# Optimization experiments

Hardware: AMD Instinct MI355X
Metric: run time of the kernel (lower is better)

The kernel has to match this reference:

```python
import jax, jax.numpy as jnp
from jax import lax
import numpy as np

EPS = 1e-5
BONES = [(0,1),(0,2),(1,3),(2,4),(5,7),(7,9),(6,8),(8,10),(11,13),(13,15),(12,14),(14,16)]


def _build_adj(num_joints=17):
    adj = np.eye(num_joints, dtype=np.float32)
    for i, j in BONES:
        adj[i, j] = 1.0
        adj[j, i] = 1.0
    d = adj.sum(1) ** -0.5
    return jnp.asarray(d[:, None] * adj * d[None, :])


def _bn(x, gamma, beta, axes):
    # training-mode BatchNorm: biased variance over `axes`
    mean = x.mean(axes, keepdims=True)
    var = ((x - mean) ** 2).mean(axes, keepdims=True)
    return (x - mean) * lax.rsqrt(var + EPS) * gamma + beta


def _gcn_block(x, adj, w, b, gamma, beta):
    # x: [N, V, Cin]; adjacency mixing then 1x1 conv (pointwise linear)
    x = jnp.einsum('nvc,vw->nwc', x, adj)
    x = jnp.einsum('nvc,oc->nvo', x, w) + b            # Conv1d(k=1): [N, V, Cout]
    x = _bn(x, gamma, beta, axes=(0, 1))               # BN over channel Cout
    return jax.nn.relu(x)


def setup_inputs() -> dict:
    key = jax.random.key(0)
    ks = jax.random.split(key, 16)
    B, T, V, C, H = 64, 512, 17, 2, 128
    s = 0.1
    return {
        'x':   jax.random.normal(ks[0], (B, T, V, C), jnp.float32),
        'adj': _build_adj(V),
        'w1':  jax.random.normal(ks[1], (64, C), jnp.float32) * s,
        'b1':  jax.random.normal(ks[2], (64,), jnp.float32) * s,
        'g1':  1.0 + jax.random.normal(ks[3], (64,), jnp.float32) * s,
        'be1': jax.random.normal(ks[4], (64,), jnp.float32) * s,
        'w2':  jax.random.normal(ks[5], (H, 64), jnp.float32) * s,
        'b2':  jax.random.normal(ks[6], (H,), jnp.float32) * s,
        'g2':  1.0 + jax.random.normal(ks[7], (H,), jnp.float32) * s,
        'be2': jax.random.normal(ks[8], (H,), jnp.float32) * s,
        'wt':  jax.random.normal(ks[9], (H, H * V, 3), jnp.float32) * 0.02,
        'bt':  jax.random.normal(ks[10], (H,), jnp.float32) * s,
        'gt':  1.0 + jax.random.normal(ks[11], (H,), jnp.float32) * s,
        'bet': jax.random.normal(ks[12], (H,), jnp.float32) * s,
    }


def reference(x, adj, w1, b1, g1, be1, w2, b2, g2, be2, wt, bt, gt, bet):
    B, T, V, C = x.shape
    h = x.reshape(B * T, V, C)
    h = _gcn_block(h, adj, w1, b1, g1, be1)            # [B*T, V, 64]
    h = _gcn_block(h, adj, w2, b2, g2, be2)            # [B*T, V, H]
    H = h.shape[-1]
    # matches torch: view(B,T,V,H).permute(0,3,1,2).contiguous().view(B,-1,T)
    h = h.reshape(B, T, V, H).transpose(0, 3, 1, 2).reshape(B, H * V, T)
    h = lax.conv_general_dilated(h, wt, (1,), [(1, 1)],
                                 dimension_numbers=('NCH', 'OIH', 'NCH'))
    h = h + bt[None, :, None]                          # [B, H, T]
    h = _bn(h, gt[None, :, None], bet[None, :, None], axes=(0, 2))
    h = jax.nn.relu(h)
    return h.transpose(0, 2, 1)                        # [B, T, H]
```

## Files before the change

kernel.cpp:

```cpp
#include <hip/hip_runtime.h>
#include <hip/hip_bf16.h>

#define EPS 1e-5f

static constexpr int Bv = 64, Tv = 512, Vv = 17, Hv = 128;
static constexpr int CHv = Hv * Vv;
static constexpr long ZBv = (long)CHv * Tv;

typedef __attribute__((ext_vector_type(8))) short short8v;
typedef __attribute__((ext_vector_type(4))) float f32x4;
typedef __attribute__((ext_vector_type(4))) int   int4v;

__device__ static const int TAPSP[17] = {
    0 | (1 << 8) | (2 << 16),
    1 | (0 << 8) | (3 << 16),
    2 | (0 << 8) | (4 << 16),
    3 | (1 << 8) | (11 << 16),
    4 | (2 << 8) | (12 << 16),
    5 | (7 << 8) | (13 << 16),
    6 | (8 << 8) | (14 << 16),
    7 | (5 << 8) | (9 << 16),
    8 | (6 << 8) | (10 << 16),
    9 | (7 << 8) | (0 << 16),
    10 | (8 << 8) | (1 << 16),
    11 | (13 << 8) | (2 << 16),
    12 | (14 << 8) | (3 << 16),
    13 | (11 << 8) | (15 << 16),
    14 | (12 << 8) | (16 << 16),
    15 | (13 << 8) | (6 << 16),
    16 | (14 << 8) | (7 << 16),
};

static constexpr size_t SZ_Z    = (size_t)Bv * (size_t)ZBv * 2;
static constexpr size_t OFF_ZR  = 0;
static constexpr size_t OFF_WKT = OFF_ZR + SZ_Z;
static constexpr size_t SZ_WKT  = (size_t)3 * 128 * 2176 * 2;
static constexpr size_t OFF_W2B = OFF_WKT + SZ_WKT;
static constexpr size_t SZ_W2B  = (size_t)128 * 64 * 2;
static constexpr size_t OFF_CP  = OFF_W2B + SZ_W2B;
static constexpr size_t SZ_CP   = (size_t)Bv * Hv * Tv * 4;
static constexpr size_t OFF_ST  = OFF_CP + SZ_CP;

__device__ __forceinline__ int4v ld16(const __hip_bfloat16* p) {
    return *reinterpret_cast<const int4v*>(p);
}
__device__ __forceinline__ f32x4 mfma16(int4v a, int4v b, f32x4 c) {
    return __builtin_amdgcn_mfma_f32_16x16x32_bf16(
        *reinterpret_cast<short8v*>(&a), *reinterpret_cast<short8v*>(&b), c, 0, 0, 0);
}
__device__ __forceinline__ float bf2f(short s) {
    return __uint_as_float(((unsigned)(unsigned short)s) << 16);
}

__global__ __launch_bounds__(256) void k_wt_bf16(const float* __restrict__ wt,
                                                 __hip_bfloat16* __restrict__ wkt2) {
    int i = blockIdx.x * 256 + threadIdx.x;
    if (i >= 3 * 128 * 2176) return;
    int el = i & 7;
    int ln = (i >> 3) & 63;
    int r  = i >> 9;
    int c  = r % 68; r /= 68;
    int oT = r & 7;  int k = r >> 3;
    int o   = oT * 16 + (ln & 15);
    int cip = c * 32 + ((ln >> 4) << 3) + el;
    int q = cip >> 7, o_in = cip & 127;
    wkt2[i] = __float2bfloat16(wt[(size_t)o * 6528 + (o_in * 17 + q) * 3 + k]);
}

__global__ __launch_bounds__(256) void k_w2b(const float* __restrict__ w2,
                                             __hip_bfloat16* __restrict__ w2b) {
    int e = blockIdx.x * 256 + threadIdx.x;
    if (e >= 8192) return;
    w2b[e] = __float2bfloat16(w2[e]);
}

__global__ __launch_bounds__(256) void k_stats1(const float* __restrict__ x,
                                                const float* __restrict__ adj,
                                                const float* __restrict__ w1,
                                                const float* __restrict__ b1,
                                                float* __restrict__ st) {
    __shared__ float adj_s[289];
    __shared__ float xs[32 * 34];
    __shared__ float mix[32 * 34];
    __shared__ float red[256], red2[256];
    int tid = threadIdx.x;
    int n0 = blockIdx.x * 32;
    for (int i = tid; i < 289; i += 256) adj_s[i] = adj[i];
    for (int i = tid; i < 1088; i += 256) xs[i] = x[(size_t)n0 * 34 + i];
    __syncthreads();
    for (int e = tid; e < 1088; e += 256) {
        int n = e / 34, r = e % 34;
        int w = r >> 1, c = r & 1;
        int pk = TAPSP[w];
        float acc = 0.f;
#pragma unroll
        for (int tp = 0; tp < 3; ++tp) {
            int v = (pk >> (8 * tp)) & 31;
            acc += xs[n * 34 + v * 2 + c] * adj_s[v * 17 + w];
        }
        mix[n * 34 + w * 2 + c] = acc;
    }
    __syncthreads();
    int o = tid & 63, g = tid >> 6;
    float w0 = w1[o * 2], w1v = w1[o * 2 + 1], bb = b1[o];
    float s = 0.f, s2 = 0.f;
    for (int n = g; n < 32; n += 4)
        for (int v = 0; v < 17; ++v) {
            float a = mix[n * 34 + v * 2] * w0 + mix[n * 34 + v * 2 + 1] * w1v + bb;
            s += a; s2 += a * a;
        }
    red[tid] = s; red2[tid] = s2;
    __syncthreads();
    if (tid < 64) {
        float S  = red[tid] + red[tid + 64] + red[tid + 128] + red[tid + 192];
        float S2 = red2[tid] + red2[tid + 64] + red2[tid + 128] + red2[tid + 192];
        int slot = blockIdx.x & 15;
        atomicAdd(&st[slot * 64 + o], S);
        atomicAdd(&st[1024 + slot * 64 + o], S2);
    }
}

__global__ void k_finalize(const float* __restrict__ sums, const float* __restrict__ sumsq,
                           const float* __restrict__ gamma, const float* __restrict__ beta,
                           float* __restrict__ scale, float* __restrict__ shift,
                           int count, float inv_denom) {
    int o = threadIdx.x;
    if (o >= count) return;
    float S = 0.f, Q = 0.f;
    for (int j = 0; j < 16; ++j) { S += sums[j * count + o]; Q += sumsq[j * count + o]; }
    float m = S * inv_denom;
    float var = Q * inv_denom - m * m;
    float rstd = rsqrtf(var + EPS);
    float sc = rstd * gamma[o];
    scale[o] = sc;
    shift[o] = beta[o] - m * sc;
}

__global__ __launch_bounds__(256) void k_gcn(const float* __restrict__ x,
                                             const float* __restrict__ adj,
                                             const float* __restrict__ w1,
                                             const float* __restrict__ b1,
                                             const float* __restrict__ sc1,
                                             const float* __restrict__ sh1,
                                             const __hip_bfloat16* __restrict__ w2b,
                                             const float* __restrict__ b2,
                                             float* __restrict__ st,
                                             __hip_bfloat16* __restrict__ zr2) {
    __shared__ float adj_s[289];
    __shared__ float xs[170];
    __shared__ float mix1[170];
    __shared__ __align__(16) char uni[26240];
    __hip_bfloat16* h1b  = reinterpret_cast<__hip_bfloat16*>(uni);
    __hip_bfloat16* m2b  = reinterpret_cast<__hip_bfloat16*>(uni + 14976);
    __hip_bfloat16* a2st = reinterpret_cast<__hip_bfloat16*>(uni);

    int tid = threadIdx.x;
    int bi = blockIdx.x;
    int b = bi / 136, rb = bi - b * 136;
    int r0 = rb * 64;
    int t_lo = r0 / 17;

    for (int i = tid; i < 289; i += 256) adj_s[i] = adj[i];
    for (int i = tid; i < 170; i += 256) {
        int tt = i / 34, r = i - tt * 34;
        int t = min(t_lo + tt, 511);
        xs[i] = x[(size_t)(b * 512 + t) * 34 + r];
    }
    __syncthreads();

    for (int e = tid; e < 170; e += 256) {
        int n = e / 34, r = e % 34, w = r >> 1, c = r & 1;
        int pk = TAPSP[w];
        float acc = 0.f;
#pragma unroll
        for (int tp = 0; tp < 3; ++tp) {
            int v = (pk >> (8 * tp)) & 31;
            acc += xs[n * 34 + v * 2 + c] * adj_s[v * 17 + w];
        }
        mix1[n * 34 + w * 2 + c] = acc;
    }
    __syncthreads();

    for (int e = tid; e < 85 * 64; e += 256) {
        int row = e >> 6, o = e & 63;
        int n = row / 17, v = row - n * 17;
        float a = mix1[n * 34 + v * 2] * w1[o * 2] + mix1[n * 34 + v * 2 + 1] * w1[o * 2 + 1] + b1[o];
        a = a * sc1[o] + sh1[o];
        h1b[row * 88 + o] = __float2bfloat16(fmaxf(a, 0.f));
    }
    __syncthreads();

    {
        int j = tid >> 2, cq = (tid & 3) << 4;
        int tv = r0 + j;
        int t = tv / 17, w = tv - t * 17;
        int base = (t - t_lo) * 17;
        int pk = TAPSP[w];
        float a[16];
#pragma unroll
        for (int i = 0; i < 16; ++i) a[i] = 0.f;
#pragma unroll
        for (int tp = 0; tp < 3; ++tp) {
            int v = (pk >> (8 * tp)) & 31;
            float ad = adj_s[v * 17 + w];
            short8v p0 = *reinterpret_cast<const short8v*>(&h1b[(base + v) * 88 + cq]);
            short8v p1 = *reinterpret_cast<const short8v*>(&h1b[(base + v) * 88 + cq + 8]);
#pragma unroll
            for (int i = 0; i < 8; ++i) {
                a[i]     += ad * bf2f(p0[i]);
                a[i + 8] += ad * bf2f(p1[i]);
            }
        }
        __hip_bfloat16* mp = &m2b[j * 88 + cq];
#pragma unroll
        for (int i = 0; i < 16; ++i) mp[i] = __float2bfloat16(a[i]);
    }
    __syncthreads();

    int wid = tid >> 6, lane = tid & 63;
    int l15 = lane & 15, l4 = lane >> 4;
    int m0 = (wid >> 1) * 64, nh = (wid & 1) * 32;

    short8v afr[4][2];
#pragma unroll
    for (int mi = 0; mi < 4; ++mi)
#pragma unroll
        for (int kk = 0; kk < 2; ++kk)
            afr[mi][kk] = *reinterpret_cast<const short8v*>(
                w2b + (size_t)(m0 + mi * 16 + l15) * 64 + kk * 32 + l4 * 8);

    f32x4 acc[4][2];
#pragma unroll
    for (int mi = 0; mi < 4; ++mi)
#pragma unroll
        for (int ni = 0; ni < 2; ++ni) acc[mi][ni] = (f32x4){0.f, 0.f, 0.f, 0.f};

#pragma unroll
    for (int kk = 0; kk < 2; ++kk)
#pragma unroll
        for (int ni = 0; ni < 2; ++ni) {
            short8v bfr = *reinterpret_cast<const short8v*>(
                &m2b[(nh + ni * 16 + l15) * 88 + kk * 32 + l4 * 8]);
#pragma unroll
            for (int mi = 0; mi < 4; ++mi)
                acc[mi][ni] = __builtin_amdgcn_mfma_f32_16x16x32_bf16(
                    afr[mi][kk], bfr, acc[mi][ni], 0, 0, 0);
        }
    __syncthreads();

#pragma unroll
    for (int mi = 0; mi < 4; ++mi)
#pragma unroll
        for (int r = 0; r < 4; ++r) {
            int o = m0 + mi * 16 + l4 * 4 + r;
            float bb = b2[o];
            a2st[(nh + l15) * 136 + o]      = __float2bfloat16(acc[mi][0][r] + bb);
            a2st[(nh + 16 + l15) * 136 + o] = __float2bfloat16(acc[mi][1][r] + bb);
        }
    __syncthreads();

    {
        int o = tid & 127, half = tid >> 7;
        float s = 0.f, q = 0.f;
        int j0 = half * 32;
#pragma unroll 8
        for (int j = j0; j < j0 + 32; ++j) {
            float v = bf2f(*reinterpret_cast<const short*>(&a2st[j * 136 + o]));
            s += v; q += v * v;
        }
        int slot = bi & 15;
        atomicAdd(&st[2048 + slot * 128 + o], s);
        atomicAdd(&st[4096 + slot * 128 + o], q);
    }

    int sf0 = r0 & 511;
    int T0 = sf0 >> 4;
    int q  = r0 >> 9;
    for (int e = tid; e < 1024; e += 256) {
        int ft = e >> 6, ln = e & 63;
        int sfti = ft >> 2, cic = ft & 3;
        int row = sfti * 16 + (ln & 15);
        int col = cic * 32 + ((ln >> 4) << 3);
        short8v val = *reinterpret_cast<const short8v*>(&a2st[row * 136 + col]);
        size_t dst = (((size_t)(b * 32 + T0 + sfti) * 68) + (q * 4 + cic)) * 512 + ln * 8;
        *reinterpret_cast<short8v*>(zr2 + dst) = val;
    }
}

__device__ __forceinline__ int4v bnrelu(int4v raw, const float* scr, const float* shr) {
    int4v out;
#pragma unroll
    for (int j = 0; j < 4; ++j) {
        unsigned w = (unsigned)raw[j];
        float lo = __uint_as_float(w << 16);
        float hi = __uint_as_float(w & 0xffff0000u);
        lo = fmaxf(lo * scr[2 * j] + shr[2 * j], 0.f);
        hi = fmaxf(hi * scr[2 * j + 1] + shr[2 * j + 1], 0.f);
        __hip_bfloat162 p = __float22bfloat162_rn(make_float2(lo, hi));
        out[j] = *reinterpret_cast<int*>(&p);
    }
    return out;
}

__global__ __launch_bounds__(256, 2) void k_conv_mfma(const __hip_bfloat16* __restrict__ zr2,
                                                      const __hip_bfloat16* __restrict__ wkt2,
                                                      const float* __restrict__ sc2,
                                                      const float* __restrict__ sh2,
                                                      const float* __restrict__ bt,
                                                      float* __restrict__ cp,
                                                      float* __restrict__ s3,
                                                      float* __restrict__ ss3) {
    __shared__ float scs[128], shs[128];
    __shared__ __align__(16) __hip_bfloat16 zbuf[2][66][40];

    int tid = threadIdx.x;
    if (tid < 128) { scs[tid] = sc2[tid]; shs[tid] = sh2[tid]; }

    int bi = blockIdx.x;
    int b  = bi >> 3;
    int sB = (bi & 7) << 6;
    int T  = sB >> 4;
    int wid = tid >> 6, lane = tid & 63;
    int l15 = lane & 15, l4 = lane >> 4;
    int m0 = (wid >> 1) * 64;
    int n0loc = (wid & 1) * 32;
    int mT = m0 >> 4;

    int sf_f = tid >> 6;
    int srow = sf_f * 16 + l15 + 1;
    int sch  = l4 * 8;
    size_t smain = ((size_t)(b * 32 + T + sf_f) * 68) * 512 + (size_t)lane * 8;
    bool has_edge = tid < 8;
    int er  = tid >> 2;
    int elg = tid & 3;
    int esf = sB - 1 + er * 65;
    bool eok = (unsigned)esf < 512u;
    int erow = er * 65;
    size_t sedge = eok ? (((size_t)(b * 32 + (esf >> 4)) * 68) * 512
                          + (size_t)((elg * 16 + (esf & 15)) * 8)) : 0;

    int aoffE[3][4];
#pragma unroll
    for (int k = 0; k < 3; ++k)
#pragma unroll
        for (int mi = 0; mi < 4; ++mi)
            aoffE[k][mi] = ((k * 8 + mT + mi) * 68) * 512 + lane * 8;

    f32x4 acc[4][2];
#pragma unroll
    for (int mi = 0; mi < 4; ++mi)
#pragma unroll
        for (int ni = 0; ni < 2; ++ni) acc[mi][ni] = (f32x4){0.f, 0.f, 0.f, 0.f};

    __syncthreads();

    {
        int4v mr = ld16(zr2 + smain);
        float scr[8], shr[8];
        *reinterpret_cast<f32x4*>(scr)     = *reinterpret_cast<const f32x4*>(&scs[sch]);
        *reinterpret_cast<f32x4*>(scr + 4) = *reinterpret_cast<const f32x4*>(&scs[sch + 4]);
        *reinterpret_cast<f32x4*>(shr)     = *reinterpret_cast<const f32x4*>(&shs[sch]);
        *reinterpret_cast<f32x4*>(shr + 4) = *reinterpret_cast<const f32x4*>(&shs[sch + 4]);
        *reinterpret_cast<int4v*>(&zbuf[0][srow][sch]) = bnrelu(mr, scr, shr);
        if (has_edge) {
            int4v ev = (int4v){0, 0, 0, 0};
            if (eok) {
                int4v erv = ld16(zr2 + sedge);
                float escr[8], eshr[8];
                int ei = elg * 8;
                *reinterpret_cast<f32x4*>(escr)     = *reinterpret_cast<const f32x4*>(&scs[ei]);
                *reinterpret_cast<f32x4*>(escr + 4) = *reinterpret_cast<const f32x4*>(&scs[ei + 4]);
                *reinterpret_cast<f32x4*>(eshr)     = *reinterpret_cast<const f32x4*>(&shs[ei]);
                *reinterpret_cast<f32x4*>(eshr + 4) = *reinterpret_cast<const f32x4*>(&shs[ei + 4]);
                ev = bnrelu(erv, escr, eshr);
            }
            *reinterpret_cast<int4v*>(&zbuf[0][erow][elg * 8]) = ev;
        }
    }
    __syncthreads();

    int cur = 0;
    for (int c = 0; c < 68; ++c) {
        int c1 = c + 1;
        bool do_stage = c1 < 68;
        int4v mr = (int4v){0, 0, 0, 0}, erv = (int4v){0, 0, 0, 0};
        if (do_stage) {
            mr = ld16(zr2 + smain + ((size_t)c1 << 9));
            if (has_edge && eok) erv = ld16(zr2 + sedge + ((size_t)c1 << 9));
        }
        int4v a_[3][4];
#pragma unroll
        for (int k = 0; k < 3; ++k)
#pragma unroll
            for (int mi = 0; mi < 4; ++mi)
                a_[k][mi] = ld16(wkt2 + (size_t)aoffE[k][mi] + ((size_t)c << 9));
        int4v bf[3][2];
#pragma unroll
        for (int k = 0; k < 3; ++k)
#pragma unroll
            for (int ni = 0; ni < 2; ++ni) {
                int row = n0loc + 1 + ni * 16 + l15 + k - 1;
                bf[k][ni] = *reinterpret_cast<const int4v*>(&zbuf[cur][row][l4 * 8]);
            }
        __builtin_amdgcn_sched_barrier(0);
#pragma unroll
        for (int k = 0; k < 3; ++k)
#pragma unroll
            for (int mi = 0; mi < 4; ++mi)
#pragma unroll
                for (int ni = 0; ni < 2; ++ni)
                    acc[mi][ni] = mfma16(a_[k][mi], bf[k][ni], acc[mi][ni]);
        if (do_stage) {
            int ph = (c1 & 3) << 5;
            float scr[8], shr[8];
            *reinterpret_cast<f32x4*>(scr)     = *reinterpret_cast<const f32x4*>(&scs[ph + sch]);
            *reinterpret_cast<f32x4*>(scr + 4) = *reinterpret_cast<const f32x4*>(&scs[ph + sch + 4]);
            *reinterpret_cast<f32x4*>(shr)     = *reinterpret_cast<const f32x4*>(&shs[ph + sch]);
            *reinterpret_cast<f32x4*>(shr + 4) = *reinterpret_cast<const f32x4*>(&shs[ph + sch + 4]);
            *reinterpret_cast<int4v*>(&zbuf[cur ^ 1][srow][sch]) = bnrelu(mr, scr, shr);
            if (has_edge) {
                int4v ev = (int4v){0, 0, 0, 0};
                if (eok) {
                    int ei = ph + elg * 8;
                    float escr[8], eshr[8];
                    *reinterpret_cast<f32x4*>(escr)     = *reinterpret_cast<const f32x4*>(&scs[ei]);
                    *reinterpret_cast<f32x4*>(escr + 4) = *reinterpret_cast<const f32x4*>(&scs[ei + 4]);
                    *reinterpret_cast<f32x4*>(eshr)     = *reinterpret_cast<const f32x4*>(&shs[ei]);
                    *reinterpret_cast<f32x4*>(eshr + 4) = *reinterpret_cast<const f32x4*>(&shs[ei + 4]);
                    ev = bnrelu(erv, escr, eshr);
                }
                *reinterpret_cast<int4v*>(&zbuf[cur ^ 1][erow][elg * 8]) = ev;
            }
        }
        __syncthreads();
        cur ^= 1;
    }

    int slot = bi & 15;
#pragma unroll
    for (int mi = 0; mi < 4; ++mi)
#pragma unroll
        for (int r = 0; r < 4; ++r) {
            int o = m0 + mi * 16 + l4 * 4 + r;
            float btv = bt[o];
            float v0 = acc[mi][0][r] + btv;
            float v1 = acc[mi][1][r] + btv;
            size_t cb = ((size_t)(b * 128 + o)) * 512 + sB + n0loc + l15;
            cp[cb] = v0;
            cp[cb + 16] = v1;
            float sv = v0 + v1;
            float sq = v0 * v0 + v1 * v1;
#pragma unroll
            for (int off = 1; off < 16; off <<= 1) {
                sv += __shfl_xor(sv, off, 64);
                sq += __shfl_xor(sq, off, 64);
            }
            if (l15 == 0) {
                atomicAdd(&s3[slot * 128 + o], sv);
                atomicAdd(&ss3[slot * 128 + o], sq);
            }
        }
}

__global__ __launch_bounds__(256) void k_out(const float* __restrict__ cp,
                                             const float* __restrict__ sc3,
                                             const float* __restrict__ sh3,
                                             float* __restrict__ out) {
    __shared__ float tile[128 * 33];
    int tid = threadIdx.x;
    int b = blockIdx.x >> 4;
    int t0 = (blockIdx.x & 15) * 32;
    for (int e = tid; e < 128 * 32; e += 256) {
        int o = e >> 5, tj = e & 31;
        tile[o * 33 + tj] = cp[((size_t)b * 128 + o) * 512 + t0 + tj];
    }
    __syncthreads();
    for (int e = tid; e < 128 * 32; e += 256) {
        int o = e & 127, th = e >> 7;
        float v = tile[o * 33 + th] * sc3[o] + sh3[o];
        out[((size_t)b * 512 + t0 + th) * 128 + o] = fmaxf(v, 0.f);
    }
}

extern "C" void kernel_launch(void* const* d_in, const int* in_sizes, int n_in,
                              void* d_out, int out_size, void* d_ws, size_t ws_size,
                              hipStream_t stream) {
    const float* x   = (const float*)d_in[0];
    const float* adj = (const float*)d_in[1];
    const float* w1  = (const float*)d_in[2];
    const float* b1  = (const float*)d_in[3];
    const float* g1  = (const float*)d_in[4];
    const float* be1 = (const float*)d_in[5];
    const float* w2  = (const float*)d_in[6];
    const float* b2  = (const float*)d_in[7];
    const float* g2  = (const float*)d_in[8];
    const float* be2 = (const float*)d_in[9];
    const float* wt  = (const float*)d_in[10];
    const float* bt  = (const float*)d_in[11];
    const float* gt  = (const float*)d_in[12];
    const float* bet = (const float*)d_in[13];
    float* out = (float*)d_out;

    char* ws = (char*)d_ws;
    __hip_bfloat16* zr2  = (__hip_bfloat16*)(ws + OFF_ZR);
    __hip_bfloat16* wkt2 = (__hip_bfloat16*)(ws + OFF_WKT);
    __hip_bfloat16* w2b  = (__hip_bfloat16*)(ws + OFF_W2B);
    float* cp = (float*)(ws + OFF_CP);
    float* st = (float*)(ws + OFF_ST);

    hipMemsetAsync(st, 0, 10240 * sizeof(float), stream);

    k_wt_bf16<<<dim3(3264), dim3(256), 0, stream>>>(wt, wkt2);
    k_w2b<<<dim3(32), dim3(256), 0, stream>>>(w2, w2b);
    k_stats1<<<dim3(1024), dim3(256), 0, stream>>>(x, adj, w1, b1, st);
    k_finalize<<<dim3(1), dim3(128), 0, stream>>>(st, st + 1024, g1, be1,
                                                  st + 10240, st + 10304, 64, 1.f / 557056.f);
    k_gcn<<<dim3(8704), dim3(256), 0, stream>>>(x, adj, w1, b1,
                                                st + 10240, st + 10304,
                                                w2b, b2, st, zr2);
    k_finalize<<<dim3(1), dim3(128), 0, stream>>>(st + 2048, st + 4096, g2, be2,
                                                  st + 10368, st + 10496, 128, 1.f / 557056.f);
    k_conv_mfma<<<dim3(512), dim3(256), 0, stream>>>(zr2, wkt2,
                                                     st + 10368, st + 10496, bt,
                                                     cp, st + 6144, st + 8192);
    k_finalize<<<dim3(1), dim3(128), 0, stream>>>(st + 6144, st + 8192, gt, bet,
                                                  st + 10624, st + 10752, 128, 1.f / 32768.f);
    k_out<<<dim3(1024), dim3(256), 0, stream>>>(cp, st + 10624, st + 10752, out);
}
```

Baseline: 188.3 us.

## Stage four channel chunks per LDS buffer to cut barriers in conv MFMA loop

The conv kernel's K-loop now stages four 32-channel chunks into a wider LDS double buffer each iteration, so it runs 17 iterations instead of 68. This cuts __syncthreads and the stage/compute switches by four. Each thread issues four global loads at once, and edge rows use 32 threads. The cost is more LDS per block (about 35KB) and more live registers, which may lower occupancy under launch_bounds(256,2).

```diff
diff --git a/kernel.cpp b/kernel.cpp
--- a/kernel.cpp
+++ b/kernel.cpp
@@ -311,7 +311,7 @@
                                                       float* __restrict__ s3,
                                                       float* __restrict__ ss3) {
     __shared__ float scs[128], shs[128];
-    __shared__ __align__(16) __hip_bfloat16 zbuf[2][66][40];
+    __shared__ __align__(16) __hip_bfloat16 zbuf[2][66][136];
 
     int tid = threadIdx.x;
     if (tid < 128) { scs[tid] = sc2[tid]; shs[tid] = sh2[tid]; }
@@ -330,14 +330,18 @@
     int srow = sf_f * 16 + l15 + 1;
     int sch  = l4 * 8;
     size_t smain = ((size_t)(b * 32 + T + sf_f) * 68) * 512 + (size_t)lane * 8;
-    bool has_edge = tid < 8;
-    int er  = tid >> 2;
-    int elg = tid & 3;
+    bool has_edge = tid < 32;
+    int er   = tid >> 4;
+    int esub = tid & 15;
+    int ep   = esub >> 2;
+    int eg   = esub & 3;
     int esf = sB - 1 + er * 65;
     bool eok = (unsigned)esf < 512u;
     int erow = er * 65;
     size_t sedge = eok ? (((size_t)(b * 32 + (esf >> 4)) * 68) * 512
-                          + (size_t)((elg * 16 + (esf & 15)) * 8)) : 0;
+                          + (size_t)((eg * 16 + (esf & 15)) * 8)) : 0;
+    int ecol = ep * 32 + eg * 8;
+    int eci  = ep * 32 + eg * 8;
 
     int aoffE[3][4];
 #pragma unroll
@@ -355,81 +359,90 @@
     __syncthreads();
 
     {
-        int4v mr = ld16(zr2 + smain);
-        float scr[8], shr[8];
-        *reinterpret_cast<f32x4*>(scr)     = *reinterpret_cast<const f32x4*>(&scs[sch]);
-        *reinterpret_cast<f32x4*>(scr + 4) = *reinterpret_cast<const f32x4*>(&scs[sch + 4]);
-        *reinterpret_cast<f32x4*>(shr)     = *reinterpret_cast<const f32x4*>(&shs[sch]);
-        *reinterpret_cast<f32x4*>(shr + 4) = *reinterpret_cast<const f32x4*>(&shs[sch + 4]);
-        *reinterpret_cast<int4v*>(&zbuf[0][srow][sch]) = bnrelu(mr, scr, shr);
-        if (has_edge) {
-            int4v ev = (int4v){0, 0, 0, 0};
-            if (eok) {
-                int4v erv = ld16(zr2 + sedge);
-                float escr[8], eshr[8];
-                int ei = elg * 8;
-                *reinterpret_cast<f32x4*>(escr)     = *reinterpret_cast<const f32x4*>(&scs[ei]);
-                *reinterpret_cast<f32x4*>(escr + 4) = *reinterpret_cast<const f32x4*>(&scs[ei + 4]);
-                *reinterpret_cast<f32x4*>(eshr)     = *reinterpret_cast<const f32x4*>(&shs[ei]);
-                *reinterpret_cast<f32x4*>(eshr + 4) = *reinterpret_cast<const f32x4*>(&shs[ei + 4]);
-                ev = bnrelu(erv, escr, eshr);
-            }
-            *reinterpret_cast<int4v*>(&zbuf[0][erow][elg * 8]) = ev;
-        }
-    }
-    __syncthreads();
-
-    int cur = 0;
-    for (int c = 0; c < 68; ++c) {
-        int c1 = c + 1;
-        bool do_stage = c1 < 68;
-        int4v mr = (int4v){0, 0, 0, 0}, erv = (int4v){0, 0, 0, 0};
-        if (do_stage) {
-            mr = ld16(zr2 + smain + ((size_t)c1 << 9));
-            if (has_edge && eok) erv = ld16(zr2 + sedge + ((size_t)c1 << 9));
-        }
-        int4v a_[3][4];
-#pragma unroll
-        for (int k = 0; k < 3; ++k)
-#pragma unroll
-            for (int mi = 0; mi < 4; ++mi)
-                a_[k][mi] = ld16(wkt2 + (size_t)aoffE[k][mi] + ((size_t)c << 9));
-        int4v bf[3][2];
-#pragma unroll
-        for (int k = 0; k < 3; ++k)
-#pragma unroll
-            for (int ni = 0; ni < 2; ++ni) {
-                int row = n0loc + 1 + ni * 16 + l15 + k - 1;
-                bf[k][ni] = *reinterpret_cast<const int4v*>(&zbuf[cur][row][l4 * 8]);
-            }
-        __builtin_amdgcn_sched_barrier(0);
-#pragma unroll
-        for (int k = 0; k < 3; ++k)
-#pragma unroll
-            for (int mi = 0; mi < 4; ++mi)
-#pragma unroll
-                for (int ni = 0; ni < 2; ++ni)
-                    acc[mi][ni] = mfma16(a_[k][mi], bf[k][ni], acc[mi][ni]);
-        if (do_stage) {
-            int ph = (c1 & 3) << 5;
+#pragma unroll
+        for (int j = 0; j < 4; ++j) {
+            int4v mr = ld16(zr2 + smain + ((size_t)j << 9));
             float scr[8], shr[8];
+            int ph = j * 32;
             *reinterpret_cast<f32x4*>(scr)     = *reinterpret_cast<const f32x4*>(&scs[ph + sch]);
             *reinterpret_cast<f32x4*>(scr + 4) = *reinterpret_cast<const f32x4*>(&scs[ph + sch + 4]);
             *reinterpret_cast<f32x4*>(shr)     = *reinterpret_cast<const f32x4*>(&shs[ph + sch]);
             *reinterpret_cast<f32x4*>(shr + 4) = *reinterpret_cast<const f32x4*>(&shs[ph + sch + 4]);
-            *reinterpret_cast<int4v*>(&zbuf[cur ^ 1][srow][sch]) = bnrelu(mr, scr, shr);
+            *reinterpret_cast<int4v*>(&zbuf[0][srow][j * 32 + sch]) = bnrelu(mr, scr, shr);
+        }
+        if (has_edge) {
+            int4v ev = (int4v){0, 0, 0, 0};
+            if (eok) {
+                int4v erv = ld16(zr2 + sedge + ((size_t)ep << 9));
+                float escr[8], eshr[8];
+#pragma unroll
+                for (int j = 0; j < 8; ++j) { escr[j] = scs[eci + j]; eshr[j] = shs[eci + j]; }
+                ev = bnrelu(erv, escr, eshr);
+            }
+            *reinterpret_cast<int4v*>(&zbuf[0][erow][ecol]) = ev;
+        }
+    }
+    __syncthreads();
+
+    int cur = 0;
+    for (int it = 0; it < 17; ++it) {
+        int cquad = it * 4;
+        bool do_stage = it < 16;
+        int4v mrs[4];
+        int4v erv = (int4v){0, 0, 0, 0};
+#pragma unroll
+        for (int j = 0; j < 4; ++j) mrs[j] = (int4v){0, 0, 0, 0};
+        if (do_stage) {
+#pragma unroll
+            for (int j = 0; j < 4; ++j)
+                mrs[j] = ld16(zr2 + smain + ((size_t)(cquad + 4 + j) << 9));
+            if (has_edge && eok) erv = ld16(zr2 + sedge + ((size_t)(cquad + 4 + ep) << 9));
+        }
+#pragma unroll
+        for (int j = 0; j < 4; ++j) {
+            int4v a_[3][4];
+#pragma unroll
+            for (int k = 0; k < 3; ++k)
+#pragma unroll
+                for (int mi = 0; mi < 4; ++mi)
+                    a_[k][mi] = ld16(wkt2 + (size_t)aoffE[k][mi] + ((size_t)(cquad + j) << 9));
+            int4v bf[3][2];
+#pragma unroll
+            for (int k = 0; k < 3; ++k)
+#pragma unroll
+                for (int ni = 0; ni < 2; ++ni) {
+                    int row = n0loc + 1 + ni * 16 + l15 + k - 1;
+                    bf[k][ni] = *reinterpret_cast<const int4v*>(&zbuf[cur][row][j * 32 + l4 * 8]);
+                }
+            __builtin_amdgcn_sched_barrier(0);
+#pragma unroll
+            for (int k = 0; k < 3; ++k)
+#pragma unroll
+                for (int mi = 0; mi < 4; ++mi)
+#pragma unroll
+                    for (int ni = 0; ni < 2; ++ni)
+                        acc[mi][ni] = mfma16(a_[k][mi], bf[k][ni], acc[mi][ni]);
+        }
+        if (do_stage) {
+#pragma unroll
+            for (int j = 0; j < 4; ++j) {
+                float scr[8], shr[8];
+                int ph = j * 32;
+                *reinterpret_cast<f32x4*>(scr)     = *reinterpret_cast<const f32x4*>(&scs[ph + sch]);
+                *reinterpret_cast<f32x4*>(scr + 4) = *reinterpret_cast<const f32x4*>(&scs[ph + sch + 4]);
+                *reinterpret_cast<f32x4*>(shr)     = *reinterpret_cast<const f32x4*>(&shs[ph + sch]);
+                *reinterpret_cast<f32x4*>(shr + 4) = *reinterpret_cast<const f32x4*>(&shs[ph + sch + 4]);
+                *reinterpret_cast<int4v*>(&zbuf[cur ^ 1][srow][j * 32 + sch]) = bnrelu(mrs[j], scr, shr);
+            }
             if (has_edge) {
                 int4v ev = (int4v){0, 0, 0, 0};
                 if (eok) {
-                    int ei = ph + elg * 8;
                     float escr[8], eshr[8];
-                    *reinterpret_cast<f32x4*>(escr)     = *reinterpret_cast<const f32x4*>(&scs[ei]);
-                    *reinterpret_cast<f32x4*>(escr + 4) = *reinterpret_cast<const f32x4*>(&scs[ei + 4]);
-                    *reinterpret_cast<f32x4*>(eshr)     = *reinterpret_cast<const f32x4*>(&shs[ei]);
-                    *reinterpret_cast<f32x4*>(eshr + 4) = *reinterpret_cast<const f32x4*>(&shs[ei + 4]);
+#pragma unroll
+                    for (int j = 0; j < 8; ++j) { escr[j] = scs[eci + j]; eshr[j] = shs[eci + j]; }
                     ev = bnrelu(erv, escr, eshr);
                 }
-                *reinterpret_cast<int4v*>(&zbuf[cur ^ 1][erow][elg * 8]) = ev;
+                *reinterpret_cast<int4v*>(&zbuf[cur ^ 1][erow][ecol]) = ev;
             }
         }
         __syncthreads();
```

After: 184.0 us. -2.3%, faster.
